# Optimization experiments

Measured on AMD Instinct MI355X. Metric: run time of the kernel, lower is better.

## Reference

```python
import jax, jax.numpy as jnp
import numpy as np

L = 2          # TinyTransformer layers
H = 8          # heads
N_REC = 6      # num_recursions
HID, RD, AD = 1024, 512, 256


def _ln(x, g, b, eps=1e-5):
    m = jnp.mean(x, -1, keepdims=True)
    v = jnp.mean((x - m) ** 2, -1, keepdims=True)
    return (x - m) * jax.lax.rsqrt(v + eps) * g + b


def _block(x, g1, be1, wqkv, bqkv, wo, bo, g2, be2, w1, b1, w2, b2):
    # pre-LN transformer block; x: (B, S, D)
    B, S, D = x.shape
    dh = D // H
    h = _ln(x, g1, be1)
    qkv = h @ wqkv + bqkv                      # (B,S,3D)
    q, k, v = jnp.split(qkv, 3, axis=-1)
    q = q.reshape(B, S, H, dh)
    k = k.reshape(B, S, H, dh)
    v = v.reshape(B, S, H, dh)
    s = jnp.einsum('bqhd,bkhd->bhqk', q, k) / np.float32(np.sqrt(dh))
    a = jax.nn.softmax(s, axis=-1)
    o = jnp.einsum('bhqk,bkhd->bqhd', a, v).reshape(B, S, D)
    x = x + o @ wo + bo
    h = _ln(x, g2, be2)
    x = x + jax.nn.gelu(h @ w1 + b1) @ w2 + b2
    return x


def _tiny_transformer(z2d, tp):
    # TinyTransformer on a single-token sequence: (B, D) -> (B, 1, D) -> (B, D)
    x = z2d[:, None, :]
    for i in range(L):
        x = _block(x, *[t[i] for t in tp])
    return x[:, 0, :]


def setup_inputs() -> dict:
    key = jax.random.key(0)
    ks = jax.random.split(key, 20)
    s = 0.02
    d = {
        'x_encoded': jax.random.normal(ks[0], (128, 512, HID), jnp.float32),
        'y_current': jax.random.normal(ks[1], (128, AD), jnp.float32),
        'Wpi': jax.random.normal(ks[2], (HID, RD), jnp.float32) * s,
        'bpi': jnp.zeros((RD,), jnp.float32),
        'Wpa': jax.random.normal(ks[3], (AD, RD), jnp.float32) * s,
        'bpa': jnp.zeros((RD,), jnp.float32),
        'Wc': jax.random.normal(ks[4], (3 * RD, RD), jnp.float32) * s,
        'bc': jnp.zeros((RD,), jnp.float32),
        'ln1_g': jnp.ones((L, RD), jnp.float32),
        'ln1_b': jnp.zeros((L, RD), jnp.float32),
        'wqkv': jax.random.normal(ks[5], (L, RD, 3 * RD), jnp.float32) * s,
        'bqkv': jnp.zeros((L, 3 * RD), jnp.float32),
        'wo': jax.random.normal(ks[6], (L, RD, RD), jnp.float32) * s,
        'bo': jnp.zeros((L, RD), jnp.float32),
        'ln2_g': jnp.ones((L, RD), jnp.float32),
        'ln2_b': jnp.zeros((L, RD), jnp.float32),
        'w1f': jax.random.normal(ks[7], (L, RD, 4 * RD), jnp.float32) * s,
        'b1f': jnp.zeros((L, 4 * RD), jnp.float32),
        'w2f': jax.random.normal(ks[8], (L, 4 * RD, RD), jnp.float32) * s,
        'b2f': jnp.zeros((L, RD), jnp.float32),
    }
    return d


def reference(x_encoded, y_current, Wpi, bpi, Wpa, bpa, Wc, bc,
              ln1_g, ln1_b, wqkv, bqkv, wo, bo, ln2_g, ln2_b,
              w1f, b1f, w2f, b2f):
    x_pooled = jnp.mean(x_encoded, axis=1)            # (B, HID)
    x_proj = x_pooled @ Wpi + bpi                      # (B, RD)
    y_proj = y_current @ Wpa + bpa                     # (B, RD)
    z = jnp.zeros_like(x_proj)
    tp = (ln1_g, ln1_b, wqkv, bqkv, wo, bo, ln2_g, ln2_b, w1f, b1f, w2f, b2f)
    for _ in range(N_REC):
        combined = jnp.concatenate([x_proj, y_proj, z], axis=-1) @ Wc + bc
        z = z + _tiny_transformer(combined, tp)
    return z
```

## Files before the change

### kernel.cpp

```cpp
#include <hip/hip_runtime.h>
#include <math.h>

#define NWG 64

typedef __bf16 bf16x8 __attribute__((ext_vector_type(8)));
typedef __bf16 bf16x4 __attribute__((ext_vector_type(4)));
typedef float  f32x4  __attribute__((ext_vector_type(4)));
typedef unsigned long long u64;

__device__ __forceinline__ float gelu_f(float x) {
  const float k0 = 0.7978845608028654f;
  const float k1 = 0.044715f;
  float x3 = x * x * x;
  return 0.5f * x * (1.0f + tanhf(k0 * (x + k1 * x3)));
}

__device__ __forceinline__ u64 cload8(const void* p) {
  return __hip_atomic_load((u64*)p, __ATOMIC_RELAXED, __HIP_MEMORY_SCOPE_AGENT);
}
__device__ __forceinline__ void cstore_bf16(__bf16* p, __bf16 h) {
  __hip_atomic_store((short*)p, __builtin_bit_cast(short, h),
                     __ATOMIC_RELAXED, __HIP_MEMORY_SCOPE_AGENT);
}

__global__ __launch_bounds__(256) void prep_kernel(
    const float* __restrict__ xe,
    const float* __restrict__ Wpi, const float* __restrict__ Wpa,
    const float* __restrict__ Wc,  const float* __restrict__ w1f,
    const float* __restrict__ w2f, const float* __restrict__ wo,
    const float* __restrict__ wqkv, const float* __restrict__ y,
    const float* __restrict__ bqkv, const float* __restrict__ bo,
    __bf16* __restrict__ xp_b,
    __bf16* __restrict__ WpiT, __bf16* __restrict__ WpaT,
    __bf16* __restrict__ WcabT, __bf16* __restrict__ WccT,
    __bf16* __restrict__ w1T,  __bf16* __restrict__ w2T,
    __bf16* __restrict__ woT,  __bf16* __restrict__ Wv_b,
    __bf16* __restrict__ y_b,  float* __restrict__ beff)
{
  int bid = blockIdx.x;
  int tid = threadIdx.x;
  if (bid < 512) {
    int b = bid >> 2;
    int c = (bid & 3) * 256 + tid;
    const float* p = xe + (size_t)b * 512 * 1024 + c;
    float s = 0.f;
#pragma unroll 16
    for (int i = 0; i < 512; ++i) s += p[(size_t)i * 1024];
    xp_b[b * 1024 + c] = (__bf16)(s * (1.f / 512.f));
  } else if (bid < 6528) {
    int t = bid - 512;
    const float* src; __bf16* dst; int R, C;
    if      (t < 512)  {            src = Wpi;            dst = WpiT;          R = 1024; C = 512;  }
    else if (t < 640)  { t -= 512;  src = Wpa;            dst = WpaT;          R = 256;  C = 512;  }
    else if (t < 1152) { t -= 640;  src = Wc;             dst = WcabT;         R = 1024; C = 512;  }
    else if (t < 1408) { t -= 1152; src = Wc + 1024*512;  dst = WccT;          R = 512;  C = 512;  }
    else if (t < 2432) { t -= 1408; src = w1f;            dst = w1T;           R = 512;  C = 2048; }
    else if (t < 3456) { t -= 2432; src = w1f + 512*2048; dst = w1T + 1048576; R = 512;  C = 2048; }
    else if (t < 4480) { t -= 3456; src = w2f;            dst = w2T;           R = 2048; C = 512;  }
    else if (t < 5504) { t -= 4480; src = w2f + 2048*512; dst = w2T + 1048576; R = 2048; C = 512;  }
    else if (t < 5760) { t -= 5504; src = wo;             dst = woT;           R = 512;  C = 512;  }
    else               { t -= 5760; src = wo + 512*512;   dst = woT + 262144;  R = 512;  C = 512;  }
    int nbc = C / 32;
    int r0 = (t / nbc) * 32;
    int c0 = (t % nbc) * 32;
    __shared__ float tt[32][33];
    int tx = tid & 31, ty = tid >> 5;
#pragma unroll
    for (int i = 0; i < 32; i += 8)
      tt[ty + i][tx] = src[(size_t)(r0 + ty + i) * C + c0 + tx];
    __syncthreads();
#pragma unroll
    for (int i = 0; i < 32; i += 8)
      dst[(size_t)(c0 + ty + i) * R + r0 + tx] = (__bf16)tt[tx][ty + i];
  } else if (bid < 6784) {
    int e0 = ((bid - 6528) * 256 + tid) * 8;
    int l = e0 >> 18, rem = e0 & 262143;
    int m = rem >> 9, k = rem & 511;
    const float* s = wqkv + (size_t)l * 786432 + (size_t)m * 1536 + 1024 + k;
#pragma unroll
    for (int j = 0; j < 8; ++j) Wv_b[e0 + j] = (__bf16)s[j];
  } else if (bid < 6800) {
    int e0 = ((bid - 6784) * 256 + tid) * 8;
#pragma unroll
    for (int j = 0; j < 8; ++j) y_b[e0 + j] = (__bf16)y[e0 + j];
  } else {
    int b2 = bid - 6800;
    int l = b2 >> 1;
    int n = (b2 & 1) * 256 + tid;
    const float* bv = bqkv + l * 1536 + 1024;
    const float* w  = wo + (size_t)l * 262144;
    float s = bo[l * 512 + n];
#pragma unroll 8
    for (int k = 0; k < 512; ++k) s += bv[k] * w[(size_t)k * 512 + n];
    beff[l * 512 + n] = s;
  }
}

__device__ __forceinline__ void gridbar(int* cnt, int target) {
  asm volatile("s_waitcnt vmcnt(0)" ::: "memory");
  __syncthreads();
  if (threadIdx.x == 0) {
    __hip_atomic_fetch_add(cnt, 1, __ATOMIC_RELAXED, __HIP_MEMORY_SCOPE_AGENT);
    while (__hip_atomic_load(cnt, __ATOMIC_RELAXED, __HIP_MEMORY_SCOPE_AGENT) < target)
      __builtin_amdgcn_s_sleep(2);
  }
  __syncthreads();
  asm volatile("" ::: "memory");
}

template<int NT, bool COHA>
__device__ __forceinline__ void ln_stats(const __bf16* A, int bm0, float& mu, float& rsg) {
  const int K = NT * 64;
  const int tid = threadIdx.x;
  const int row = tid >> 3, j8 = tid & 7;
  const __bf16* ap = A + (size_t)(bm0 + row) * K + j8 * (K / 8);
  float s = 0.f, s2 = 0.f;
#pragma unroll
  for (int i = 0; i < K / 8; i += 4) {
    bf16x4 v;
    if (COHA) v = __builtin_bit_cast(bf16x4, cload8(ap + i));
    else      v = *(const bf16x4*)(ap + i);
#pragma unroll
    for (int j = 0; j < 4; ++j) { float f = (float)v[j]; s += f; s2 += f * f; }
  }
  s  += __shfl_xor(s, 1);  s2 += __shfl_xor(s2, 1);
  s  += __shfl_xor(s, 2);  s2 += __shfl_xor(s2, 2);
  s  += __shfl_xor(s, 4);  s2 += __shfl_xor(s2, 4);
  mu = s / (float)K;
  rsg = rsqrtf(s2 / (float)K - mu * mu + 1e-5f);
}

template<int NT, int LNMODE, bool GELU, bool COHA, bool BIAS, bool RESID,
         bool ACCUM, bool OUTF, bool OUTB, bool COHO>
__device__ __forceinline__ void gemm32(
    const __bf16* A, const __bf16* Bt, int bm0, int bn0,
    const float* lng, const float* lnb, const float* bias,
    const float* resid, const float* accum, float* outf, __bf16* outb, int ldo,
    __bf16* AL, __bf16* BL, float mu_in = 0.f, float rs_in = 0.f)
{
  const int tid = threadIdx.x;
  constexpr int K = NT * 64;
  const int row = tid >> 3;
  const int kcol = (tid & 7) * 8;

  float mu = mu_in, rsg = rs_in;
  if (LNMODE == 1) ln_stats<NT, COHA>(A, bm0, mu, rsg);

  const __bf16* Ab0 = A + (size_t)(bm0 + row) * K + kcol;
  const __bf16* Bb0 = Bt + (size_t)(bn0 + row) * K + kcol;

  u64 ra0[4], ra1[4], rb0[4], rb1[4];
  auto issue = [&](int t, int s) {
    const __bf16* ap = Ab0 + t * 64;
    const __bf16* bp = Bb0 + t * 64;
    if (COHA) { ra0[s] = cload8(ap); ra1[s] = cload8(ap + 4); }
    else      { ra0[s] = *(const u64*)ap; ra1[s] = *(const u64*)(ap + 4); }
    rb0[s] = *(const u64*)bp; rb1[s] = *(const u64*)(bp + 4);
  };
#pragma unroll
  for (int s = 0; s < 4; ++s) issue(s, s);

  f32x4 acc = {0.f, 0.f, 0.f, 0.f};
  const int wave = tid >> 6, lane = tid & 63;
  const int wr = (wave >> 1) * 16, wc = (wave & 1) * 16;
  const int lr = lane & 15, lk8 = (lane >> 4) * 8;

  for (int ttc = 0; ttc < NT / 4; ++ttc) {
#pragma unroll
    for (int ti = 0; ti < 4; ++ti) {
      const int t = ttc * 4 + ti;
      bf16x4 lo = __builtin_bit_cast(bf16x4, ra0[ti]);
      bf16x4 hi = __builtin_bit_cast(bf16x4, ra1[ti]);
      if (LNMODE != 0) {
        const int kb = t * 64 + kcol;
        f32x4 g0 = *(const f32x4*)(lng + kb);
        f32x4 g1 = *(const f32x4*)(lng + kb + 4);
        f32x4 b0 = *(const f32x4*)(lnb + kb);
        f32x4 b1 = *(const f32x4*)(lnb + kb + 4);
#pragma unroll
        for (int j = 0; j < 4; ++j) {
          lo[j] = (__bf16)(((float)lo[j] - mu) * rsg * g0[j] + b0[j]);
          hi[j] = (__bf16)(((float)hi[j] - mu) * rsg * g1[j] + b1[j]);
        }
      }
      __bf16* al = AL + (ti & 1) * 2304 + row * 72 + kcol;
      __bf16* bl = BL + (ti & 1) * 2304 + row * 72 + kcol;
      *(bf16x4*)al = lo; *(bf16x4*)(al + 4) = hi;
      *(bf16x4*)bl = __builtin_bit_cast(bf16x4, rb0[ti]);
      *(bf16x4*)(bl + 4) = __builtin_bit_cast(bf16x4, rb1[ti]);
      __syncthreads();
      if (t + 4 < NT) issue(t + 4, ti);
      const __bf16* Ar = AL + (ti & 1) * 2304 + (wr + lr) * 72;
      const __bf16* Br = BL + (ti & 1) * 2304 + (wc + lr) * 72;
      bf16x8 a0 = *(const bf16x8*)(Ar + lk8);
      bf16x8 b0v = *(const bf16x8*)(Br + lk8);
      acc = __builtin_amdgcn_mfma_f32_16x16x32_bf16(a0, b0v, acc, 0, 0, 0);
      bf16x8 a1 = *(const bf16x8*)(Ar + 32 + lk8);
      bf16x8 b1v = *(const bf16x8*)(Br + 32 + lk8);
      acc = __builtin_amdgcn_mfma_f32_16x16x32_bf16(a1, b1v, acc, 0, 0, 0);
      __syncthreads();
    }
  }

  const int er = bm0 + wr + (lane >> 4) * 4;
  const int ec = bn0 + wc + lr;
#pragma unroll
  for (int e = 0; e < 4; ++e) {
    const int r = er + e;
    float v = acc[e];
    if (BIAS)  v += bias[ec];
    if (RESID) v += resid[r * 512 + ec];
    if (GELU)  v = gelu_f(v);
    if (ACCUM) v += accum[r * 512 + ec];
    if (OUTF)  outf[r * 512 + ec] = v;
    if (OUTB) {
      __bf16 h = (__bf16)v;
      if (COHO) cstore_bf16(outb + (size_t)r * ldo + ec, h);
      else      outb[(size_t)r * ldo + ec] = h;
    }
  }
}

__global__ __launch_bounds__(256) void aux_kernel(
    const __bf16* __restrict__ woT, const __bf16* __restrict__ Wv_b,
    const __bf16* __restrict__ xp_b, const __bf16* __restrict__ y_b,
    const __bf16* __restrict__ WpiT, const __bf16* __restrict__ WpaT,
    const float* __restrict__ bpi, const float* __restrict__ bpa,
    __bf16* __restrict__ WeffT, __bf16* __restrict__ xy_b)
{
  __shared__ __bf16 AL[2 * 32 * 72];
  __shared__ __bf16 BL[2 * 32 * 72];
  int bid = blockIdx.x;
  if (bid < 512) {
    int l = bid >> 8, t = bid & 255;
    gemm32<8,0,0,0,0,0,0,0,1,0>(woT + l * 262144, Wv_b + l * 262144,
        (t >> 4) * 32, (t & 15) * 32, nullptr, nullptr, nullptr,
        nullptr, nullptr, nullptr, WeffT + l * 262144, 512, AL, BL);
  } else if (bid < 576) {
    int t = bid - 512;
    gemm32<16,0,0,0,1,0,0,0,1,0>(xp_b, WpiT, (t >> 4) * 32, (t & 15) * 32,
        nullptr, nullptr, bpi, nullptr, nullptr, nullptr, xy_b, 1024, AL, BL);
  } else {
    int t = bid - 576;
    gemm32<4,0,0,0,1,0,0,0,1,0>(y_b, WpaT, (t >> 4) * 32, (t & 15) * 32,
        nullptr, nullptr, bpa, nullptr, nullptr, nullptr, xy_b + 512, 1024, AL, BL);
  }
}

__global__ __launch_bounds__(256) void mega_kernel(
    const __bf16* __restrict__ xy_b, const __bf16* __restrict__ WcabT,
    const __bf16* __restrict__ WccT, const __bf16* __restrict__ WeffT,
    const __bf16* __restrict__ w1T, const __bf16* __restrict__ w2T,
    const float* __restrict__ bc, const float* __restrict__ beff,
    const float* __restrict__ ln1g, const float* __restrict__ ln1b,
    const float* __restrict__ ln2g, const float* __restrict__ ln2b,
    const float* __restrict__ b1f, const float* __restrict__ b2f,
    float* base_f, float* c_f, __bf16* c_b, float* x_f,
    __bf16* xb2, __bf16* xb4, __bf16* u_b, float* z_f, __bf16* z_b,
    float* out, int* bcnt)
{
  __shared__ __bf16 AL[2 * 32 * 72];
  __shared__ __bf16 BL[2 * 32 * 72];
  const int wg = blockIdx.x;
  const int xcd = wg & 7, slot = wg >> 3;
  const int bm = (slot & 3) * 32;
  const int bn = (((xcd << 1) | (slot >> 2))) * 32;
  int bar = 0;

  gemm32<16,0,0,0,1,0,0,1,1,1>(xy_b, WcabT, bm, bn, nullptr, nullptr, bc,
      nullptr, nullptr, base_f, c_b, 512, AL, BL);
  gridbar(bcnt, bar += NWG);

  for (int r = 0; r < 6; ++r) {
    if (r > 0) {
      gemm32<8,0,0,1,0,1,0,1,1,1>(z_b, WccT, bm, bn, nullptr, nullptr, nullptr,
          base_f, nullptr, c_f, c_b, 512, AL, BL);
      gridbar(bcnt, bar += NWG);
    }
    for (int l = 0; l < 2; ++l) {
      const __bf16* Ain = (l == 0) ? c_b : xb4;
      const float*  Rin = (l == 0) ? ((r > 0) ? c_f : base_f) : x_f;
      gemm32<8,1,0,1,1,1,0,1,1,1>(Ain, WeffT + l * 262144, bm, bn,
          ln1g + l * 512, ln1b + l * 512, beff + l * 512, Rin, nullptr,
          x_f, xb2, 512, AL, BL);
      gridbar(bcnt, bar += NWG);
      {
        float mu, rsg;
        ln_stats<8, true>(xb2, bm, mu, rsg);
        for (int i = 0; i < 4; ++i) {
          int n3 = (xcd << 3) | ((slot >> 2) << 2) | i;
          gemm32<8,2,1,1,1,0,0,0,1,1>(xb2, w1T + l * 1048576, bm, n3 * 32,
              ln2g + l * 512, ln2b + l * 512, b1f + l * 2048, nullptr, nullptr,
              nullptr, u_b, 2048, AL, BL, mu, rsg);
        }
      }
      gridbar(bcnt, bar += NWG);
      if (l == 0) {
        gemm32<32,0,0,1,1,1,0,1,1,1>(u_b, w2T, bm, bn, nullptr, nullptr, b2f,
            x_f, nullptr, x_f, xb4, 512, AL, BL);
        gridbar(bcnt, bar += NWG);
      } else {
        if (r == 0) {
          gemm32<32,0,0,1,1,1,0,1,1,1>(u_b, w2T + 1048576, bm, bn, nullptr, nullptr,
              b2f + 512, x_f, nullptr, z_f, z_b, 512, AL, BL);
        } else if (r < 5) {
          gemm32<32,0,0,1,1,1,1,1,1,1>(u_b, w2T + 1048576, bm, bn, nullptr, nullptr,
              b2f + 512, x_f, z_f, z_f, z_b, 512, AL, BL);
        } else {
          gemm32<32,0,0,1,1,1,1,1,0,0>(u_b, w2T + 1048576, bm, bn, nullptr, nullptr,
              b2f + 512, x_f, z_f, out, nullptr, 512, AL, BL);
        }
        if (r < 5) gridbar(bcnt, bar += NWG);
      }
    }
  }
}

extern "C" void kernel_launch(void* const* d_in, const int* in_sizes, int n_in,
                              void* d_out, int out_size, void* d_ws, size_t ws_size,
                              hipStream_t stream) {
  const float* x_encoded = (const float*)d_in[0];
  const float* y_current = (const float*)d_in[1];
  const float* Wpi  = (const float*)d_in[2];
  const float* bpi  = (const float*)d_in[3];
  const float* Wpa  = (const float*)d_in[4];
  const float* bpa  = (const float*)d_in[5];
  const float* Wc   = (const float*)d_in[6];
  const float* bc   = (const float*)d_in[7];
  const float* ln1g = (const float*)d_in[8];
  const float* ln1b = (const float*)d_in[9];
  const float* wqkv = (const float*)d_in[10];
  const float* bqkv = (const float*)d_in[11];
  const float* wo   = (const float*)d_in[12];
  const float* bo   = (const float*)d_in[13];
  const float* ln2g = (const float*)d_in[14];
  const float* ln2b = (const float*)d_in[15];
  const float* w1f  = (const float*)d_in[16];
  const float* b1f  = (const float*)d_in[17];
  const float* w2f  = (const float*)d_in[18];
  const float* b2f  = (const float*)d_in[19];
  (void)in_sizes; (void)n_in; (void)out_size; (void)ws_size;

  char* wsb = (char*)d_ws;
  size_t off = 0;
  auto carve = [&](size_t bytes) -> void* {
    void* p = wsb + off;
    off += (bytes + 255) & ~(size_t)255;
    return p;
  };
  __bf16* xp_b    = (__bf16*)carve(131072 * 2);
  __bf16* y_b     = (__bf16*)carve(32768 * 2);
  __bf16* WpiT    = (__bf16*)carve(524288 * 2);
  __bf16* WpaT    = (__bf16*)carve(131072 * 2);
  __bf16* WcabT   = (__bf16*)carve(524288 * 2);
  __bf16* WccT    = (__bf16*)carve(262144 * 2);
  __bf16* w1T     = (__bf16*)carve(2097152 * 2);
  __bf16* w2T     = (__bf16*)carve(2097152 * 2);
  __bf16* woT     = (__bf16*)carve(524288 * 2);
  __bf16* Wv_b    = (__bf16*)carve(524288 * 2);
  __bf16* WeffT   = (__bf16*)carve(524288 * 2);
  float*  beff    = (float*) carve(1024 * 4);
  __bf16* xy_b    = (__bf16*)carve(131072 * 2);
  float*  base_f  = (float*) carve(65536 * 4);
  float*  c_f     = (float*) carve(65536 * 4);
  __bf16* c_b     = (__bf16*)carve(65536 * 2);
  float*  x_f     = (float*) carve(65536 * 4);
  __bf16* xb2     = (__bf16*)carve(65536 * 2);
  __bf16* xb4     = (__bf16*)carve(65536 * 2);
  __bf16* u_b     = (__bf16*)carve(262144 * 2);
  float*  z_f     = (float*) carve(65536 * 4);
  __bf16* z_b     = (__bf16*)carve(65536 * 2);
  int*    d_bar   = (int*)   carve(256);

  hipMemsetAsync(d_bar, 0, 256, stream);
  prep_kernel<<<6804, 256, 0, stream>>>(x_encoded, Wpi, Wpa, Wc, w1f, w2f, wo,
      wqkv, y_current, bqkv, bo, xp_b, WpiT, WpaT, WcabT, WccT, w1T, w2T, woT,
      Wv_b, y_b, beff);
  aux_kernel<<<640, 256, 0, stream>>>(woT, Wv_b, xp_b, y_b, WpiT, WpaT,
      bpi, bpa, WeffT, xy_b);
  mega_kernel<<<NWG, 256, 0, stream>>>(
      xy_b, WcabT, WccT, WeffT, w1T, w2T, bc, beff,
      ln1g, ln1b, ln2g, ln2b, b1f, b2f,
      base_f, c_f, c_b, x_f, xb2, xb4, u_b, z_f, z_b,
      (float*)d_out, d_bar);
}
```

Measured before the change: 550.6 us.

## Split mega kernel into row-group barriers with register-resident wave GEMMs

Replaces the 64-workgroup global grid barrier with per-group barriers: the batch is split into 4 row groups of 32 rows, each handled by 16 workgroups that sync only among themselves through slot flags and a release word. GEMMs in the recurrent loop now run per wave with 16x16 tiles, keeping the full A row slice (K=512) in registers with layernorm applied in-register, and drop LDS staging and block-level syncs. The goal is to shrink barrier latency and synchronisation overhead on the serial recurrence. In exchange, each wave re-reads its B weights from global memory with no LDS reuse, register pressure rises, and the barrier buffer grows.

```diff
diff --git a/kernel.cpp b/kernel.cpp
--- a/kernel.cpp
+++ b/kernel.cpp
@@ -1,12 +1,11 @@
 #include <hip/hip_runtime.h>
 #include <math.h>
-
-#define NWG 64
 
 typedef __bf16 bf16x8 __attribute__((ext_vector_type(8)));
 typedef __bf16 bf16x4 __attribute__((ext_vector_type(4)));
 typedef float  f32x4  __attribute__((ext_vector_type(4)));
 typedef unsigned long long u64;
+typedef u64 u64x2 __attribute__((ext_vector_type(2)));
 
 __device__ __forceinline__ float gelu_f(float x) {
   const float k0 = 0.7978845608028654f;
@@ -96,56 +95,17 @@
   }
 }
 
-__device__ __forceinline__ void gridbar(int* cnt, int target) {
-  asm volatile("s_waitcnt vmcnt(0)" ::: "memory");
-  __syncthreads();
-  if (threadIdx.x == 0) {
-    __hip_atomic_fetch_add(cnt, 1, __ATOMIC_RELAXED, __HIP_MEMORY_SCOPE_AGENT);
-    while (__hip_atomic_load(cnt, __ATOMIC_RELAXED, __HIP_MEMORY_SCOPE_AGENT) < target)
-      __builtin_amdgcn_s_sleep(2);
-  }
-  __syncthreads();
-  asm volatile("" ::: "memory");
-}
-
-template<int NT, bool COHA>
-__device__ __forceinline__ void ln_stats(const __bf16* A, int bm0, float& mu, float& rsg) {
-  const int K = NT * 64;
-  const int tid = threadIdx.x;
-  const int row = tid >> 3, j8 = tid & 7;
-  const __bf16* ap = A + (size_t)(bm0 + row) * K + j8 * (K / 8);
-  float s = 0.f, s2 = 0.f;
-#pragma unroll
-  for (int i = 0; i < K / 8; i += 4) {
-    bf16x4 v;
-    if (COHA) v = __builtin_bit_cast(bf16x4, cload8(ap + i));
-    else      v = *(const bf16x4*)(ap + i);
-#pragma unroll
-    for (int j = 0; j < 4; ++j) { float f = (float)v[j]; s += f; s2 += f * f; }
-  }
-  s  += __shfl_xor(s, 1);  s2 += __shfl_xor(s2, 1);
-  s  += __shfl_xor(s, 2);  s2 += __shfl_xor(s2, 2);
-  s  += __shfl_xor(s, 4);  s2 += __shfl_xor(s2, 4);
-  mu = s / (float)K;
-  rsg = rsqrtf(s2 / (float)K - mu * mu + 1e-5f);
-}
-
-template<int NT, int LNMODE, bool GELU, bool COHA, bool BIAS, bool RESID,
-         bool ACCUM, bool OUTF, bool OUTB, bool COHO>
+template<int NT, bool BIAS>
 __device__ __forceinline__ void gemm32(
     const __bf16* A, const __bf16* Bt, int bm0, int bn0,
-    const float* lng, const float* lnb, const float* bias,
-    const float* resid, const float* accum, float* outf, __bf16* outb, int ldo,
-    __bf16* AL, __bf16* BL, float mu_in = 0.f, float rs_in = 0.f)
+    const float* bias, __bf16* outb, int ldo,
+    __bf16* AL, __bf16* BL)
 {
   const int tid = threadIdx.x;
   constexpr int K = NT * 64;
   const int row = tid >> 3;
   const int kcol = (tid & 7) * 8;
 
-  float mu = mu_in, rsg = rs_in;
-  if (LNMODE == 1) ln_stats<NT, COHA>(A, bm0, mu, rsg);
-
   const __bf16* Ab0 = A + (size_t)(bm0 + row) * K + kcol;
   const __bf16* Bb0 = Bt + (size_t)(bn0 + row) * K + kcol;
 
@@ -153,8 +113,7 @@
   auto issue = [&](int t, int s) {
     const __bf16* ap = Ab0 + t * 64;
     const __bf16* bp = Bb0 + t * 64;
-    if (COHA) { ra0[s] = cload8(ap); ra1[s] = cload8(ap + 4); }
-    else      { ra0[s] = *(const u64*)ap; ra1[s] = *(const u64*)(ap + 4); }
+    ra0[s] = *(const u64*)ap; ra1[s] = *(const u64*)(ap + 4);
     rb0[s] = *(const u64*)bp; rb1[s] = *(const u64*)(bp + 4);
   };
 #pragma unroll
@@ -169,25 +128,10 @@
 #pragma unroll
     for (int ti = 0; ti < 4; ++ti) {
       const int t = ttc * 4 + ti;
-      bf16x4 lo = __builtin_bit_cast(bf16x4, ra0[ti]);
-      bf16x4 hi = __builtin_bit_cast(bf16x4, ra1[ti]);
-      if (LNMODE != 0) {
-        const int kb = t * 64 + kcol;
-        f32x4 g0 = *(const f32x4*)(lng + kb);
-        f32x4 g1 = *(const f32x4*)(lng + kb + 4);
-        f32x4 b0 = *(const f32x4*)(lnb + kb);
-        f32x4 b1 = *(const f32x4*)(lnb + kb + 4);
-#pragma unroll
-        for (int j = 0; j < 4; ++j) {
-          lo[j] = (__bf16)(((float)lo[j] - mu) * rsg * g0[j] + b0[j]);
-          hi[j] = (__bf16)(((float)hi[j] - mu) * rsg * g1[j] + b1[j]);
-        }
-      }
       __bf16* al = AL + (ti & 1) * 2304 + row * 72 + kcol;
       __bf16* bl = BL + (ti & 1) * 2304 + row * 72 + kcol;
-      *(bf16x4*)al = lo; *(bf16x4*)(al + 4) = hi;
-      *(bf16x4*)bl = __builtin_bit_cast(bf16x4, rb0[ti]);
-      *(bf16x4*)(bl + 4) = __builtin_bit_cast(bf16x4, rb1[ti]);
+      *(u64*)al = ra0[ti]; *(u64*)(al + 4) = ra1[ti];
+      *(u64*)bl = rb0[ti]; *(u64*)(bl + 4) = rb1[ti];
       __syncthreads();
       if (t + 4 < NT) issue(t + 4, ti);
       const __bf16* Ar = AL + (ti & 1) * 2304 + (wr + lr) * 72;
@@ -206,18 +150,9 @@
   const int ec = bn0 + wc + lr;
 #pragma unroll
   for (int e = 0; e < 4; ++e) {
-    const int r = er + e;
     float v = acc[e];
-    if (BIAS)  v += bias[ec];
-    if (RESID) v += resid[r * 512 + ec];
-    if (GELU)  v = gelu_f(v);
-    if (ACCUM) v += accum[r * 512 + ec];
-    if (OUTF)  outf[r * 512 + ec] = v;
-    if (OUTB) {
-      __bf16 h = (__bf16)v;
-      if (COHO) cstore_bf16(outb + (size_t)r * ldo + ec, h);
-      else      outb[(size_t)r * ldo + ec] = h;
-    }
+    if (BIAS) v += bias[ec];
+    outb[(size_t)(er + e) * ldo + ec] = (__bf16)v;
   }
 }
 
@@ -233,17 +168,164 @@
   int bid = blockIdx.x;
   if (bid < 512) {
     int l = bid >> 8, t = bid & 255;
-    gemm32<8,0,0,0,0,0,0,0,1,0>(woT + l * 262144, Wv_b + l * 262144,
-        (t >> 4) * 32, (t & 15) * 32, nullptr, nullptr, nullptr,
-        nullptr, nullptr, nullptr, WeffT + l * 262144, 512, AL, BL);
+    gemm32<8, false>(woT + l * 262144, Wv_b + l * 262144,
+        (t >> 4) * 32, (t & 15) * 32, nullptr, WeffT + l * 262144, 512, AL, BL);
   } else if (bid < 576) {
     int t = bid - 512;
-    gemm32<16,0,0,0,1,0,0,0,1,0>(xp_b, WpiT, (t >> 4) * 32, (t & 15) * 32,
-        nullptr, nullptr, bpi, nullptr, nullptr, nullptr, xy_b, 1024, AL, BL);
+    gemm32<16, true>(xp_b, WpiT, (t >> 4) * 32, (t & 15) * 32,
+        bpi, xy_b, 1024, AL, BL);
   } else {
     int t = bid - 576;
-    gemm32<4,0,0,0,1,0,0,0,1,0>(y_b, WpaT, (t >> 4) * 32, (t & 15) * 32,
-        nullptr, nullptr, bpa, nullptr, nullptr, nullptr, xy_b + 512, 1024, AL, BL);
+    gemm32<4, true>(y_b, WpaT, (t >> 4) * 32, (t & 15) * 32,
+        bpa, xy_b + 512, 1024, AL, BL);
+  }
+}
+
+__device__ __forceinline__ void groupbar(int* slots, int* rel, int lg, int ep) {
+  asm volatile("s_waitcnt vmcnt(0)" ::: "memory");
+  __syncthreads();
+  const int tid = threadIdx.x;
+  if (lg == 0) {
+    if (tid >= 1 && tid < 16) {
+      while (__hip_atomic_load(slots + tid * 32, __ATOMIC_RELAXED, __HIP_MEMORY_SCOPE_AGENT) < ep)
+        __builtin_amdgcn_s_sleep(1);
+    }
+    __syncthreads();
+    if (tid == 0)
+      __hip_atomic_store(rel, ep, __ATOMIC_RELAXED, __HIP_MEMORY_SCOPE_AGENT);
+  } else {
+    if (tid == 0) {
+      __hip_atomic_store(slots + lg * 32, ep, __ATOMIC_RELAXED, __HIP_MEMORY_SCOPE_AGENT);
+      while (__hip_atomic_load(rel, __ATOMIC_RELAXED, __HIP_MEMORY_SCOPE_AGENT) < ep)
+        __builtin_amdgcn_s_sleep(1);
+    }
+  }
+  __syncthreads();
+}
+
+template<int LN, int COHA, int NTILE, int GELU_, int BIAS_, int RESID_, int ACCUM_,
+         int OUTF_, int OUTB_>
+__device__ __forceinline__ void gemm_reg16(
+    const __bf16* __restrict__ A, const __bf16* __restrict__ Bt,
+    int am0, int bn0, int bnstep,
+    const float* __restrict__ lng, const float* __restrict__ lnb,
+    const float* __restrict__ bias, const float* __restrict__ resid,
+    const float* __restrict__ accum, float* __restrict__ outf,
+    __bf16* __restrict__ outb, int ldo)
+{
+  const int lane = threadIdx.x & 63;
+  const int kof = (lane >> 4) * 8;
+  const __bf16* ap = A + (size_t)(am0 + (lane & 15)) * 512 + kof;
+  bf16x8 a[16];
+#pragma unroll
+  for (int t = 0; t < 16; ++t) {
+    if (COHA) {
+      u64x2 q; q.x = cload8(ap + t * 32); q.y = cload8(ap + t * 32 + 4);
+      a[t] = __builtin_bit_cast(bf16x8, q);
+    } else {
+      a[t] = *(const bf16x8*)(ap + t * 32);
+    }
+  }
+  if (LN) {
+    float s = 0.f, s2 = 0.f;
+#pragma unroll
+    for (int t = 0; t < 16; ++t)
+#pragma unroll
+      for (int j = 0; j < 8; ++j) { float f = (float)a[t][j]; s += f; s2 += f * f; }
+    s += __shfl_xor(s, 16); s2 += __shfl_xor(s2, 16);
+    s += __shfl_xor(s, 32); s2 += __shfl_xor(s2, 32);
+    float mu = s * (1.f / 512.f);
+    float rsg = rsqrtf(s2 * (1.f / 512.f) - mu * mu + 1e-5f);
+#pragma unroll
+    for (int t = 0; t < 16; ++t) {
+      const int kb = t * 32 + kof;
+      f32x4 g0 = *(const f32x4*)(lng + kb);
+      f32x4 g1 = *(const f32x4*)(lng + kb + 4);
+      f32x4 b0 = *(const f32x4*)(lnb + kb);
+      f32x4 b1 = *(const f32x4*)(lnb + kb + 4);
+#pragma unroll
+      for (int j = 0; j < 4; ++j) {
+        a[t][j]     = (__bf16)(((float)a[t][j]     - mu) * rsg * g0[j] + b0[j]);
+        a[t][j + 4] = (__bf16)(((float)a[t][j + 4] - mu) * rsg * g1[j] + b1[j]);
+      }
+    }
+  }
+  for (int nt = 0; nt < NTILE; ++nt) {
+    const int cb = bn0 + nt * bnstep;
+    const __bf16* bp = Bt + (size_t)(cb + (lane & 15)) * 512 + kof;
+    bf16x8 b[16];
+#pragma unroll
+    for (int t = 0; t < 16; ++t) b[t] = *(const bf16x8*)(bp + t * 32);
+    f32x4 acc = {0.f, 0.f, 0.f, 0.f};
+#pragma unroll
+    for (int t = 0; t < 16; ++t)
+      acc = __builtin_amdgcn_mfma_f32_16x16x32_bf16(a[t], b[t], acc, 0, 0, 0);
+    const int col = cb + (lane & 15);
+    const int row0 = am0 + (lane >> 4) * 4;
+#pragma unroll
+    for (int e = 0; e < 4; ++e) {
+      const int r = row0 + e;
+      float v = acc[e];
+      if (BIAS_)  v += bias[col];
+      if (RESID_) v += resid[r * 512 + col];
+      if (GELU_)  v = gelu_f(v);
+      if (ACCUM_) v += accum[r * 512 + col];
+      if (OUTF_)  outf[r * 512 + col] = v;
+      if (OUTB_)  cstore_bf16(outb + (size_t)r * ldo + col, (__bf16)v);
+    }
+  }
+}
+
+template<int KS, int COHA, int BIAS_, int RESID_, int ACCUM_, int OUTF_, int OUTB_>
+__device__ __forceinline__ void gemm_stream(
+    const __bf16* __restrict__ A, const __bf16* __restrict__ Bt,
+    int am0, int bn0,
+    const float* __restrict__ bias, const float* __restrict__ resid,
+    const float* __restrict__ accum, float* __restrict__ outf,
+    __bf16* __restrict__ outb, int ldo)
+{
+  const int lane = threadIdx.x & 63;
+  const int kof = (lane >> 4) * 8;
+  constexpr int K = KS * 32;
+  const __bf16* ap = A + (size_t)(am0 + (lane & 15)) * K + kof;
+  const __bf16* bp = Bt + (size_t)(bn0 + (lane & 15)) * K + kof;
+  bf16x8 ra[8], rb[8];
+#pragma unroll
+  for (int s = 0; s < 8; ++s) {
+    if (COHA) {
+      u64x2 q; q.x = cload8(ap + s * 32); q.y = cload8(ap + s * 32 + 4);
+      ra[s] = __builtin_bit_cast(bf16x8, q);
+    } else {
+      ra[s] = *(const bf16x8*)(ap + s * 32);
+    }
+    rb[s] = *(const bf16x8*)(bp + s * 32);
+  }
+  f32x4 acc = {0.f, 0.f, 0.f, 0.f};
+#pragma unroll
+  for (int t = 0; t < KS; ++t) {
+    acc = __builtin_amdgcn_mfma_f32_16x16x32_bf16(ra[t & 7], rb[t & 7], acc, 0, 0, 0);
+    if (t + 8 < KS) {
+      const int u = t + 8;
+      if (COHA) {
+        u64x2 q; q.x = cload8(ap + u * 32); q.y = cload8(ap + u * 32 + 4);
+        ra[t & 7] = __builtin_bit_cast(bf16x8, q);
+      } else {
+        ra[t & 7] = *(const bf16x8*)(ap + u * 32);
+      }
+      rb[t & 7] = *(const bf16x8*)(bp + u * 32);
+    }
+  }
+  const int col = bn0 + (lane & 15);
+  const int row0 = am0 + (lane >> 4) * 4;
+#pragma unroll
+  for (int e = 0; e < 4; ++e) {
+    const int r = row0 + e;
+    float v = acc[e];
+    if (BIAS_)  v += bias[col];
+    if (RESID_) v += resid[r * 512 + col];
+    if (ACCUM_) v += accum[r * 512 + col];
+    if (OUTF_)  outf[r * 512 + col] = v;
+    if (OUTB_)  cstore_bf16(outb + (size_t)r * ldo + col, (__bf16)v);
   }
 }
 
@@ -257,60 +339,53 @@
     const float* __restrict__ b1f, const float* __restrict__ b2f,
     float* base_f, float* c_f, __bf16* c_b, float* x_f,
     __bf16* xb2, __bf16* xb4, __bf16* u_b, float* z_f, __bf16* z_b,
-    float* out, int* bcnt)
-{
-  __shared__ __bf16 AL[2 * 32 * 72];
-  __shared__ __bf16 BL[2 * 32 * 72];
+    float* out, int* bar)
+{
   const int wg = blockIdx.x;
-  const int xcd = wg & 7, slot = wg >> 3;
-  const int bm = (slot & 3) * 32;
-  const int bn = (((xcd << 1) | (slot >> 2))) * 32;
-  int bar = 0;
-
-  gemm32<16,0,0,0,1,0,0,1,1,1>(xy_b, WcabT, bm, bn, nullptr, nullptr, bc,
-      nullptr, nullptr, base_f, c_b, 512, AL, BL);
-  gridbar(bcnt, bar += NWG);
+  const int g = wg >> 4, lg = wg & 15;
+  const int wv = lg * 4 + (threadIdx.x >> 6);
+  const int sr = wv >> 5, ct = wv & 31;
+  const int am0 = g * 32 + sr * 16;
+  const int bn = ct * 16;
+  int* slots = bar + g * 512;
+  int* rel   = bar + 2048 + g * 32;
+  int ep = 0;
+
+  gemm_stream<32, 0, 1, 0, 0, 1, 1>(xy_b, WcabT, am0, bn, bc, nullptr, nullptr,
+                                    base_f, c_b, 512);
+  groupbar(slots, rel, lg, ++ep);
 
   for (int r = 0; r < 6; ++r) {
     if (r > 0) {
-      gemm32<8,0,0,1,0,1,0,1,1,1>(z_b, WccT, bm, bn, nullptr, nullptr, nullptr,
-          base_f, nullptr, c_f, c_b, 512, AL, BL);
-      gridbar(bcnt, bar += NWG);
+      gemm_reg16<0, 1, 1, 0, 0, 1, 0, 1, 1>(z_b, WccT, am0, bn, 0,
+          nullptr, nullptr, nullptr, base_f, nullptr, c_f, c_b, 512);
+      groupbar(slots, rel, lg, ++ep);
     }
     for (int l = 0; l < 2; ++l) {
       const __bf16* Ain = (l == 0) ? c_b : xb4;
       const float*  Rin = (l == 0) ? ((r > 0) ? c_f : base_f) : x_f;
-      gemm32<8,1,0,1,1,1,0,1,1,1>(Ain, WeffT + l * 262144, bm, bn,
-          ln1g + l * 512, ln1b + l * 512, beff + l * 512, Rin, nullptr,
-          x_f, xb2, 512, AL, BL);
-      gridbar(bcnt, bar += NWG);
-      {
-        float mu, rsg;
-        ln_stats<8, true>(xb2, bm, mu, rsg);
-        for (int i = 0; i < 4; ++i) {
-          int n3 = (xcd << 3) | ((slot >> 2) << 2) | i;
-          gemm32<8,2,1,1,1,0,0,0,1,1>(xb2, w1T + l * 1048576, bm, n3 * 32,
-              ln2g + l * 512, ln2b + l * 512, b1f + l * 2048, nullptr, nullptr,
-              nullptr, u_b, 2048, AL, BL, mu, rsg);
-        }
-      }
-      gridbar(bcnt, bar += NWG);
+      const int lo = l * 512;
+      gemm_reg16<1, 1, 1, 0, 1, 1, 0, 1, 1>(Ain, WeffT + l * 262144, am0, bn, 0,
+          ln1g + lo, ln1b + lo, beff + lo, Rin, nullptr, x_f, xb2, 512);
+      groupbar(slots, rel, lg, ++ep);
+      gemm_reg16<1, 1, 4, 1, 1, 0, 0, 0, 1>(xb2, w1T + l * 1048576, am0, bn, 512,
+          ln2g + lo, ln2b + lo, b1f + l * 2048, nullptr, nullptr, nullptr, u_b, 2048);
+      groupbar(slots, rel, lg, ++ep);
       if (l == 0) {
-        gemm32<32,0,0,1,1,1,0,1,1,1>(u_b, w2T, bm, bn, nullptr, nullptr, b2f,
-            x_f, nullptr, x_f, xb4, 512, AL, BL);
-        gridbar(bcnt, bar += NWG);
+        gemm_stream<64, 1, 1, 1, 0, 1, 1>(u_b, w2T, am0, bn, b2f, x_f, nullptr,
+                                          x_f, xb4, 512);
+        groupbar(slots, rel, lg, ++ep);
+      } else if (r == 0) {
+        gemm_stream<64, 1, 1, 1, 0, 1, 1>(u_b, w2T + 1048576, am0, bn, b2f + 512,
+                                          x_f, nullptr, z_f, z_b, 512);
+        groupbar(slots, rel, lg, ++ep);
+      } else if (r < 5) {
+        gemm_stream<64, 1, 1, 1, 1, 1, 1>(u_b, w2T + 1048576, am0, bn, b2f + 512,
+                                          x_f, z_f, z_f, z_b, 512);
+        groupbar(slots, rel, lg, ++ep);
       } else {
-        if (r == 0) {
-          gemm32<32,0,0,1,1,1,0,1,1,1>(u_b, w2T + 1048576, bm, bn, nullptr, nullptr,
-              b2f + 512, x_f, nullptr, z_f, z_b, 512, AL, BL);
-        } else if (r < 5) {
-          gemm32<32,0,0,1,1,1,1,1,1,1>(u_b, w2T + 1048576, bm, bn, nullptr, nullptr,
-              b2f + 512, x_f, z_f, z_f, z_b, 512, AL, BL);
-        } else {
-          gemm32<32,0,0,1,1,1,1,1,0,0>(u_b, w2T + 1048576, bm, bn, nullptr, nullptr,
-              b2f + 512, x_f, z_f, out, nullptr, 512, AL, BL);
-        }
-        if (r < 5) gridbar(bcnt, bar += NWG);
+        gemm_stream<64, 1, 1, 1, 1, 1, 0>(u_b, w2T + 1048576, am0, bn, b2f + 512,
+                                          x_f, z_f, out, nullptr, 512);
       }
     }
   }
@@ -370,15 +445,15 @@
   __bf16* u_b     = (__bf16*)carve(262144 * 2);
   float*  z_f     = (float*) carve(65536 * 4);
   __bf16* z_b     = (__bf16*)carve(65536 * 2);
-  int*    d_bar   = (int*)   carve(256);
-
-  hipMemsetAsync(d_bar, 0, 256, stream);
+  int*    d_bar   = (int*)   carve(16384);
+
+  hipMemsetAsync(d_bar, 0, 16384, stream);
   prep_kernel<<<6804, 256, 0, stream>>>(x_encoded, Wpi, Wpa, Wc, w1f, w2f, wo,
       wqkv, y_current, bqkv, bo, xp_b, WpiT, WpaT, WcabT, WccT, w1T, w2T, woT,
       Wv_b, y_b, beff);
   aux_kernel<<<640, 256, 0, stream>>>(woT, Wv_b, xp_b, y_b, WpiT, WpaT,
       bpi, bpa, WeffT, xy_b);
-  mega_kernel<<<NWG, 256, 0, stream>>>(
+  mega_kernel<<<64, 256, 0, stream>>>(
       xy_b, WcabT, WccT, WeffT, w1T, w2T, bc, beff,
       ln1g, ln1b, ln2g, ln2b, b1f, b2f,
       base_f, c_f, c_b, x_f, xb2, xb4, u_b, z_f, z_b,
```

Measured after the change: 742.6 us. 34.9% more time.
